# Optimization experiments

Hardware: AMD Instinct MI355X
Metric: run time of the kernel (lower is better)

## Reference

```python
import jax, jax.numpy as jnp
import numpy as np

N_NODES = 50000
D_IN = 256
D_OUT = 128
N_POS = 1600000   # positive edges used for GCN aggregation
N_PRED = 500000   # edges to score


def setup_inputs() -> dict:
    key = jax.random.key(0)
    ks = jax.random.split(key, 6)
    x = jax.random.normal(ks[0], (N_NODES, D_IN), dtype=jnp.float32)
    pos_edge_index = jax.random.randint(ks[1], (2, N_POS), 0, N_NODES)
    edge_index = jax.random.randint(ks[2], (2, N_PRED), 0, N_NODES)
    # init_linear: Linear(d_in, d_in); stored as (in, out) so fwd is x @ W1 + b1
    W1 = jax.random.normal(ks[3], (D_IN, D_IN), dtype=jnp.float32) / np.sqrt(D_IN).astype(np.float32)
    b1 = jnp.zeros((D_IN,), dtype=jnp.float32)
    # GCNConv weight (in, out) and bias
    Wc = jax.random.normal(ks[4], (D_IN, D_OUT), dtype=jnp.float32) / np.sqrt(D_IN).astype(np.float32)
    bc = jnp.zeros((D_OUT,), dtype=jnp.float32)
    return dict(x=x, edge_index=edge_index, pos_edge_index=pos_edge_index,
                W1=W1, b1=b1, Wc=Wc, bc=bc)


def reference(x, edge_index, pos_edge_index, W1, b1, Wc, bc):
    n = x.shape[0]
    # init_linear
    h = x @ W1 + b1                                  # [N, D_IN]
    # GCNConv: linear transform first, then normalized scatter-add aggregation
    h = h @ Wc                                       # [N, D_OUT]
    # add self-loops (PyG GCNConv default add_self_loops=True, edge_weight=1)
    loops = jnp.arange(n, dtype=pos_edge_index.dtype)
    row = jnp.concatenate([pos_edge_index[0], loops])  # source
    col = jnp.concatenate([pos_edge_index[1], loops])  # target (aggregation)
    # symmetric normalization: deg over target, norm = d^-1/2[row]*d^-1/2[col]
    deg = jax.ops.segment_sum(jnp.ones_like(col, dtype=h.dtype), col, num_segments=n)
    dinv = jnp.where(deg > 0, jax.lax.rsqrt(deg), 0.0)
    norm = dinv[row] * dinv[col]                     # [E+N]
    msgs = h[row] * norm[:, None]                    # gather + scale
    out = jax.ops.segment_sum(msgs, col, num_segments=n) + bc  # scatter-add + bias
    # edge dot-product scoring
    logits = (out[edge_index[0]] * out[edge_index[1]]).sum(axis=-1)  # [N_PRED]
    return logits
```

## Files before the change

### kernel.cpp

```cpp
#include <hip/hip_runtime.h>

#define N_NODES 50000
#define D_IN 256
#define D_OUT 128
#define N_POS 1600000
#define N_PRED 500000

#define G_BUCKETS 782
#define GPAD 1024
#define SB 640
#define CHUNK 2500
#define CAP 4096
#define GEMM_BLOCKS 782
#define QPRED 125000

typedef __attribute__((ext_vector_type(8))) short short8;
typedef __attribute__((ext_vector_type(4))) float f32x4;

__device__ __forceinline__ unsigned short f2bf(float f) {
    unsigned int u = __float_as_uint(f);
    u += 0x7FFFu + ((u >> 16) & 1u);
    return (unsigned short)(u >> 16);
}
__device__ __forceinline__ unsigned int pk2(float a, float b) {
    unsigned int ua = __float_as_uint(a), ub = __float_as_uint(b);
    ua += 0x7FFFu + ((ua >> 16) & 1u);
    ub += 0x7FFFu + ((ub >> 16) & 1u);
    return (ua >> 16) | (ub & 0xFFFF0000u);
}
__device__ __forceinline__ float bflo(unsigned int u) { return __uint_as_float(u << 16); }
__device__ __forceinline__ float bfhi(unsigned int u) { return __uint_as_float(u & 0xFFFF0000u); }

__device__ __forceinline__ float dot8(uint4 ua, uint4 ub) {
    return bflo(ua.x) * bflo(ub.x) + bfhi(ua.x) * bfhi(ub.x)
         + bflo(ua.y) * bflo(ub.y) + bfhi(ua.y) * bfhi(ub.y)
         + bflo(ua.z) * bflo(ub.z) + bfhi(ua.z) * bfhi(ub.z)
         + bflo(ua.w) * bflo(ub.w) + bfhi(ua.w) * bfhi(ub.w);
}

__global__ void fuse_weights_k(const float* __restrict__ W1, const float* __restrict__ Wc,
                               const float* __restrict__ b1,
                               unsigned short* __restrict__ Bp, float* __restrict__ bf,
                               int* __restrict__ bfill) {
    if (blockIdx.x == 128) {
        for (int g = threadIdx.x; g < G_BUCKETS; g += 256) bfill[g] = g * CAP;
        return;
    }
    int gid = blockIdx.x * blockDim.x + threadIdx.x;
    int k = gid >> 7;
    int n = gid & 127;
    float acc = 0.f;
    #pragma unroll 4
    for (int kk = 0; kk < D_IN; ++kk)
        acc += W1[k * D_IN + kk] * Wc[kk * D_OUT + n];
    int ks = k >> 5, q = (k >> 3) & 3, jj = k & 7;
    int nt = n >> 4, nl = n & 15;
    int lane = q * 16 + nl;
    Bp[(((long)(ks * 8 + nt)) * 64 + lane) * 8 + jj] = f2bf(acc);
    if (gid < D_OUT) {
        float accb = 0.f;
        for (int kk = 0; kk < D_IN; ++kk)
            accb += b1[kk] * Wc[kk * D_OUT + gid];
        bf[gid] = accb;
    }
}

__global__ __launch_bounds__(256) void scatter_gemm_k(const int* __restrict__ row,
                                                      const int* __restrict__ col,
                                                      int* __restrict__ bfill,
                                                      unsigned int* __restrict__ eb,
                                                      const float* __restrict__ x,
                                                      const uint4* __restrict__ Bp,
                                                      const float* __restrict__ bf,
                                                      unsigned short* __restrict__ hsb) {
    __shared__ __align__(16) char smem[27456];
    if (blockIdx.x < GEMM_BLOCKS) {
        const int wave = threadIdx.x >> 6;
        const int lane = threadIdx.x & 63;
        const int q    = lane >> 4;
        const int ml   = lane & 15;
        const int m0   = blockIdx.x * 64 + wave * 16;

        f32x4 acc[8];
        #pragma unroll
        for (int t = 0; t < 8; ++t) acc[t] = (f32x4){0.f, 0.f, 0.f, 0.f};

        long arow = m0 + ml; if (arow > N_NODES - 1) arow = N_NODES - 1;
        const float* xrow = x + arow * D_IN + q * 8;

        #pragma unroll
        for (int ks = 0; ks < 8; ++ks) {
            float4 xa = *(const float4*)(xrow + ks * 32);
            float4 xb = *(const float4*)(xrow + ks * 32 + 4);
            union { short8 s; unsigned int u[4]; } af;
            af.u[0] = pk2(xa.x, xa.y);
            af.u[1] = pk2(xa.z, xa.w);
            af.u[2] = pk2(xb.x, xb.y);
            af.u[3] = pk2(xb.z, xb.w);
            #pragma unroll
            for (int nt = 0; nt < 8; ++nt) {
                union { uint4 v; short8 s; } bu;
                bu.v = Bp[(long)(ks * 8 + nt) * 64 + lane];
                acc[nt] = __builtin_amdgcn_mfma_f32_16x16x32_bf16(af.s, bu.s, acc[nt], 0, 0, 0);
            }
        }

        unsigned short* o = (unsigned short*)smem + wave * 2048;
        #pragma unroll
        for (int nt = 0; nt < 8; ++nt) {
            float bn = bf[nt * 16 + ml];
            #pragma unroll
            for (int r = 0; r < 4; ++r) {
                float val = acc[nt][r] + bn;
                o[(q * 4 + r) * 128 + nt * 16 + ml] = f2bf(val);
            }
        }
        __syncthreads();
        #pragma unroll
        for (int i = 0; i < 4; ++i) {
            int fb = i * 1024 + lane * 16;
            int v = m0 + (fb >> 8);
            if (v < N_NODES) {
                uint4 val = *(const uint4*)((const char*)o + fb);
                *(uint4*)((char*)hsb + (long)v * 256 + (fb & 255)) = val;
            }
        }
    } else {
        int* hist  = (int*)smem;
        int* lofs  = hist + GPAD;
        int* fill2 = lofs + GPAD;
        int* base  = fill2 + GPAD;
        int* part  = base + GPAD;
        unsigned int* stag = (unsigned int*)(part + 256);
        int t = threadIdx.x;
        for (int i = t; i < GPAD; i += 256) { hist[i] = 0; fill2[i] = 0; }
        __syncthreads();
        int e0 = (blockIdx.x - GEMM_BLOCKS) * CHUNK;
        for (int i = t; i < CHUNK; i += 256)
            atomicAdd(&hist[col[e0 + i] >> 6], 1);
        __syncthreads();
        int h[4], p4 = 0;
        #pragma unroll
        for (int i = 0; i < 4; ++i) { h[i] = hist[4 * t + i]; p4 += h[i]; }
        part[t] = p4;
        __syncthreads();
        for (int d = 1; d < 256; d <<= 1) {
            int add = (t >= d) ? part[t - d] : 0;
            __syncthreads();
            part[t] += add;
            __syncthreads();
        }
        int ex = part[t] - p4;
        #pragma unroll
        for (int i = 0; i < 4; ++i) { lofs[4 * t + i] = ex; ex += h[i]; }
        __syncthreads();
        for (int g = t; g < G_BUCKETS; g += 256) {
            int c = hist[g];
            base[g] = c ? atomicAdd(&bfill[g], c) : 0;
        }
        for (int i = t; i < CHUNK; i += 256) {
            int c = col[e0 + i];
            int g = c >> 6;
            unsigned int u = (unsigned int)row[e0 + i] | ((unsigned int)(c & 63) << 16)
                           | ((unsigned int)g << 22);
            int lp = atomicAdd(&fill2[g], 1);
            stag[lofs[g] + lp] = u;
        }
        __syncthreads();
        for (int i = t; i < CHUNK; i += 256) {
            unsigned int u = stag[i];
            int g = u >> 22;
            eb[base[g] + (i - lofs[g])] = u;
        }
    }
}

__global__ __launch_bounds__(256) void csr_build_k(const int* __restrict__ bfill,
                                                   const unsigned int* __restrict__ eb,
                                                   unsigned short* __restrict__ csr,
                                                   int* __restrict__ offs,
                                                   int* __restrict__ ends,
                                                   float* __restrict__ dinv) {
    __shared__ unsigned int stag[CAP];
    __shared__ unsigned short stag2[CAP];
    __shared__ int hist[64], lofs[64], fill[64];
    int t = threadIdx.x;
    int g = blockIdx.x;
    int s = g * CAP;
    int cnt = bfill[g] - s;
    if (t < 64) { hist[t] = 0; fill[t] = 0; }
    __syncthreads();
    for (int i = t; i < cnt; i += 256) {
        unsigned int u = eb[s + i];
        stag[i] = u;
        atomicAdd(&hist[(u >> 16) & 63], 1);
    }
    __syncthreads();
    if (t == 0) {
        int run = 0;
        for (int k = 0; k < 64; ++k) { lofs[k] = run; run += hist[k]; }
    }
    __syncthreads();
    if (t < 64) {
        int v = g * 64 + t;
        if (v < N_NODES) {
            offs[v] = s + lofs[t];
            ends[v] = s + lofs[t] + hist[t];
            dinv[v] = rsqrtf((float)hist[t] + 1.0f);
        }
    }
    for (int i = t; i < cnt; i += 256) {
        unsigned int u = stag[i];
        int nl = (u >> 16) & 63;
        int lp = atomicAdd(&fill[nl], 1);
        stag2[lofs[nl] + lp] = (unsigned short)(u & 0xFFFF);
    }
    __syncthreads();
    for (int i = t; i < cnt; i += 256)
        csr[s + i] = stag2[i];
}

__global__ __launch_bounds__(256) void aggregate_csr_k(const int* __restrict__ offs,
                                                       const int* __restrict__ ends,
                                                       const unsigned short* __restrict__ csr,
                                                       const uint4* __restrict__ hs4,
                                                       const float* __restrict__ dinv,
                                                       const float* __restrict__ bc,
                                                       uint4* __restrict__ feat4) {
    int v    = blockIdx.x * 4 + (threadIdx.x >> 6);
    int lane = threadIdx.x & 63;
    int grp  = lane >> 4, li = lane & 15;
    int s0 = offs[v], s1 = ends[v];

    float a[8] = {0.f, 0.f, 0.f, 0.f, 0.f, 0.f, 0.f, 0.f};
    int i = s0 + grp;
    for (; i + 12 < s1; i += 16) {
        int r0 = csr[i], r1 = csr[i + 4], r2 = csr[i + 8], r3 = csr[i + 12];
        uint4 u0 = hs4[r0 * 16 + li];
        uint4 u1 = hs4[r1 * 16 + li];
        uint4 u2 = hs4[r2 * 16 + li];
        uint4 u3 = hs4[r3 * 16 + li];
        float d0 = dinv[r0], d1 = dinv[r1], d2 = dinv[r2], d3 = dinv[r3];
        a[0] = fmaf(d0, bflo(u0.x), a[0]); a[0] = fmaf(d1, bflo(u1.x), a[0]);
        a[0] = fmaf(d2, bflo(u2.x), a[0]); a[0] = fmaf(d3, bflo(u3.x), a[0]);
        a[1] = fmaf(d0, bfhi(u0.x), a[1]); a[1] = fmaf(d1, bfhi(u1.x), a[1]);
        a[1] = fmaf(d2, bfhi(u2.x), a[1]); a[1] = fmaf(d3, bfhi(u3.x), a[1]);
        a[2] = fmaf(d0, bflo(u0.y), a[2]); a[2] = fmaf(d1, bflo(u1.y), a[2]);
        a[2] = fmaf(d2, bflo(u2.y), a[2]); a[2] = fmaf(d3, bflo(u3.y), a[2]);
        a[3] = fmaf(d0, bfhi(u0.y), a[3]); a[3] = fmaf(d1, bfhi(u1.y), a[3]);
        a[3] = fmaf(d2, bfhi(u2.y), a[3]); a[3] = fmaf(d3, bfhi(u3.y), a[3]);
        a[4] = fmaf(d0, bflo(u0.z), a[4]); a[4] = fmaf(d1, bflo(u1.z), a[4]);
        a[4] = fmaf(d2, bflo(u2.z), a[4]); a[4] = fmaf(d3, bflo(u3.z), a[4]);
        a[5] = fmaf(d0, bfhi(u0.z), a[5]); a[5] = fmaf(d1, bfhi(u1.z), a[5]);
        a[5] = fmaf(d2, bfhi(u2.z), a[5]); a[5] = fmaf(d3, bfhi(u3.z), a[5]);
        a[6] = fmaf(d0, bflo(u0.w), a[6]); a[6] = fmaf(d1, bflo(u1.w), a[6]);
        a[6] = fmaf(d2, bflo(u2.w), a[6]); a[6] = fmaf(d3, bflo(u3.w), a[6]);
        a[7] = fmaf(d0, bfhi(u0.w), a[7]); a[7] = fmaf(d1, bfhi(u1.w), a[7]);
        a[7] = fmaf(d2, bfhi(u2.w), a[7]); a[7] = fmaf(d3, bfhi(u3.w), a[7]);
    }
    for (; i + 4 < s1; i += 8) {
        int r0 = csr[i], r1 = csr[i + 4];
        uint4 u0 = hs4[r0 * 16 + li];
        uint4 u1 = hs4[r1 * 16 + li];
        float d0 = dinv[r0], d1 = dinv[r1];
        a[0] = fmaf(d0, bflo(u0.x), a[0]); a[0] = fmaf(d1, bflo(u1.x), a[0]);
        a[1] = fmaf(d0, bfhi(u0.x), a[1]); a[1] = fmaf(d1, bfhi(u1.x), a[1]);
        a[2] = fmaf(d0, bflo(u0.y), a[2]); a[2] = fmaf(d1, bflo(u1.y), a[2]);
        a[3] = fmaf(d0, bfhi(u0.y), a[3]); a[3] = fmaf(d1, bfhi(u1.y), a[3]);
        a[4] = fmaf(d0, bflo(u0.z), a[4]); a[4] = fmaf(d1, bflo(u1.z), a[4]);
        a[5] = fmaf(d0, bfhi(u0.z), a[5]); a[5] = fmaf(d1, bfhi(u1.z), a[5]);
        a[6] = fmaf(d0, bflo(u0.w), a[6]); a[6] = fmaf(d1, bflo(u1.w), a[6]);
        a[7] = fmaf(d0, bfhi(u0.w), a[7]); a[7] = fmaf(d1, bfhi(u1.w), a[7]);
    }
    if (i < s1) {
        int r = csr[i];
        uint4 u = hs4[r * 16 + li];
        float d = dinv[r];
        a[0] = fmaf(d, bflo(u.x), a[0]); a[1] = fmaf(d, bfhi(u.x), a[1]);
        a[2] = fmaf(d, bflo(u.y), a[2]); a[3] = fmaf(d, bfhi(u.y), a[3]);
        a[4] = fmaf(d, bflo(u.z), a[4]); a[5] = fmaf(d, bfhi(u.z), a[5]);
        a[6] = fmaf(d, bflo(u.w), a[6]); a[7] = fmaf(d, bfhi(u.w), a[7]);
    }
    #pragma unroll
    for (int j = 0; j < 8; ++j) {
        a[j] += __shfl_xor(a[j], 16);
        a[j] += __shfl_xor(a[j], 32);
    }
    if (grp == 0) {
        uint4 su = hs4[v * 16 + li];
        float dv = dinv[v];
        float4 b0 = *(const float4*)(bc + li * 8);
        float4 b1 = *(const float4*)(bc + li * 8 + 4);
        float f0 = dv * (a[0] + dv * bflo(su.x)) + b0.x;
        float f1 = dv * (a[1] + dv * bfhi(su.x)) + b0.y;
        float f2 = dv * (a[2] + dv * bflo(su.y)) + b0.z;
        float f3 = dv * (a[3] + dv * bfhi(su.y)) + b0.w;
        float f4 = dv * (a[4] + dv * bflo(su.z)) + b1.x;
        float f5 = dv * (a[5] + dv * bfhi(su.z)) + b1.y;
        float f6 = dv * (a[6] + dv * bflo(su.w)) + b1.z;
        float f7 = dv * (a[7] + dv * bfhi(su.w)) + b1.w;
        uint4 o;
        o.x = pk2(f0, f1); o.y = pk2(f2, f3); o.z = pk2(f4, f5); o.w = pk2(f6, f7);
        feat4[v * 16 + li] = o;
    }
}

__global__ void score_k(const int* __restrict__ src, const int* __restrict__ dst,
                        const uint4* __restrict__ feat4, float* __restrict__ out) {
    int gid = blockIdx.x * blockDim.x + threadIdx.x;
    int e = gid >> 4;
    int c = gid & 15;
    if (e >= QPRED) return;
    int e0 = e, e1 = e + QPRED, e2 = e + 2 * QPRED, e3 = e + 3 * QPRED;
    int a0 = src[e0], b0 = dst[e0];
    int a1 = src[e1], b1 = dst[e1];
    int a2 = src[e2], b2 = dst[e2];
    int a3 = src[e3], b3 = dst[e3];
    uint4 ua0 = feat4[(long)a0 * 16 + c];
    uint4 ub0 = feat4[(long)b0 * 16 + c];
    uint4 ua1 = feat4[(long)a1 * 16 + c];
    uint4 ub1 = feat4[(long)b1 * 16 + c];
    uint4 ua2 = feat4[(long)a2 * 16 + c];
    uint4 ub2 = feat4[(long)b2 * 16 + c];
    uint4 ua3 = feat4[(long)a3 * 16 + c];
    uint4 ub3 = feat4[(long)b3 * 16 + c];
    float p0 = dot8(ua0, ub0);
    float p1 = dot8(ua1, ub1);
    float p2 = dot8(ua2, ub2);
    float p3 = dot8(ua3, ub3);
    #pragma unroll
    for (int m = 8; m; m >>= 1) {
        p0 += __shfl_xor(p0, m, 16);
        p1 += __shfl_xor(p1, m, 16);
        p2 += __shfl_xor(p2, m, 16);
        p3 += __shfl_xor(p3, m, 16);
    }
    if (c == 0) {
        out[e0] = p0;
        out[e1] = p1;
        out[e2] = p2;
        out[e3] = p3;
    }
}

extern "C" void kernel_launch(void* const* d_in, const int* in_sizes, int n_in,
                              void* d_out, int out_size, void* d_ws, size_t ws_size,
                              hipStream_t stream) {
    const float* x   = (const float*)d_in[0];
    const int*   ei  = (const int*)  d_in[1];
    const int*   pe  = (const int*)  d_in[2];
    const float* W1  = (const float*)d_in[3];
    const float* b1  = (const float*)d_in[4];
    const float* Wc  = (const float*)d_in[5];
    const float* bc  = (const float*)d_in[6];
    float* out = (float*)d_out;

    const int* pe_row = pe;
    const int* pe_col = pe + N_POS;
    const int* ei_src = ei;
    const int* ei_dst = ei + N_PRED;

    char* w = (char*)d_ws;
    unsigned short* Bp = (unsigned short*)w;  w += 32768 * 2;
    float* bf    = (float*)w;                 w += 128 * 4;
    float* dinv  = (float*)w;                 w += 50000 * 4;
    int*   bfill = (int*)w;                   w += GPAD * 4;
    int*   offs  = (int*)w;                   w += 50000 * 4;
    int*   ends  = (int*)w;                   w += 50000 * 4;
    unsigned int* eb = (unsigned int*)w;      w += (long)G_BUCKETS * CAP * 4;
    unsigned short* csr = (unsigned short*)w; w += (long)G_BUCKETS * CAP * 2;
    unsigned short* hsb   = (unsigned short*)w;  w += (long)N_NODES * D_OUT * 2;
    unsigned short* featb = (unsigned short*)w;

    fuse_weights_k<<<129, 256, 0, stream>>>(W1, Wc, b1, Bp, bf, bfill);

    scatter_gemm_k<<<GEMM_BLOCKS + SB, 256, 0, stream>>>(pe_row, pe_col, bfill, eb,
                                                         x, (const uint4*)Bp, bf, hsb);

    csr_build_k   <<<G_BUCKETS, 256, 0, stream>>>(bfill, eb, csr, offs, ends, dinv);

    aggregate_csr_k<<<N_NODES / 4, 256, 0, stream>>>(offs, ends, csr, (const uint4*)hsb,
                                                     dinv, bc, (uint4*)featb);

    score_k       <<<(QPRED * 16 + 255) / 256, 256, 0, stream>>>(
                      ei_src, ei_dst, (const uint4*)featb, out);
}
```

Measured before the change: 264.7 us.

## Partition CSR neighbor lists by source tile for cache-local aggregation

The CSR build now sorts each node's neighbors into four source-row tiles and records five offsets per node. The aggregation kernel processes 25 nodes per block and sweeps the tiles in order, keeping partial sums in shared memory. The aim is to keep the gathered hs rows within a smaller working set so they hit in cache. In exchange it adds a parallel prefix scan in the CSR build, per-tile loop overhead, shared-memory accumulation and a lower per-wave unroll depth.

```diff
diff --git a/kernel.cpp b/kernel.cpp
--- a/kernel.cpp
+++ b/kernel.cpp
@@ -13,6 +13,11 @@
 #define CAP 4096
 #define GEMM_BLOCKS 782
 #define QPRED 125000
+
+#define NT 4
+#define TSZ 12500
+#define NPB 25
+#define AGGB 2000
 
 typedef __attribute__((ext_vector_type(8))) short short8;
 typedef __attribute__((ext_vector_type(4))) float f32x4;
@@ -178,130 +183,141 @@
 __global__ __launch_bounds__(256) void csr_build_k(const int* __restrict__ bfill,
                                                    const unsigned int* __restrict__ eb,
                                                    unsigned short* __restrict__ csr,
-                                                   int* __restrict__ offs,
-                                                   int* __restrict__ ends,
+                                                   int* __restrict__ offs5,
                                                    float* __restrict__ dinv) {
     __shared__ unsigned int stag[CAP];
     __shared__ unsigned short stag2[CAP];
-    __shared__ int hist[64], lofs[64], fill[64];
+    __shared__ int hist[256], lofs[256], fill[256], part[256];
     int t = threadIdx.x;
     int g = blockIdx.x;
     int s = g * CAP;
     int cnt = bfill[g] - s;
-    if (t < 64) { hist[t] = 0; fill[t] = 0; }
+    hist[t] = 0; fill[t] = 0;
     __syncthreads();
     for (int i = t; i < cnt; i += 256) {
         unsigned int u = eb[s + i];
         stag[i] = u;
-        atomicAdd(&hist[(u >> 16) & 63], 1);
-    }
-    __syncthreads();
-    if (t == 0) {
-        int run = 0;
-        for (int k = 0; k < 64; ++k) { lofs[k] = run; run += hist[k]; }
-    }
+        int r = u & 0xFFFF;
+        int tile = (r >= TSZ) + (r >= 2 * TSZ) + (r >= 3 * TSZ);
+        atomicAdd(&hist[((u >> 16) & 63) * NT + tile], 1);
+    }
+    __syncthreads();
+    int hv = hist[t];
+    part[t] = hv;
+    __syncthreads();
+    for (int d = 1; d < 256; d <<= 1) {
+        int add = (t >= d) ? part[t - d] : 0;
+        __syncthreads();
+        part[t] += add;
+        __syncthreads();
+    }
+    lofs[t] = part[t] - hv;
     __syncthreads();
     if (t < 64) {
         int v = g * 64 + t;
         if (v < N_NODES) {
-            offs[v] = s + lofs[t];
-            ends[v] = s + lofs[t] + hist[t];
-            dinv[v] = rsqrtf((float)hist[t] + 1.0f);
+            int b4 = t * NT;
+            int o0 = s + lofs[b4];
+            int c0 = hist[b4], c1 = hist[b4 + 1], c2 = hist[b4 + 2], c3 = hist[b4 + 3];
+            offs5[v * 5 + 0] = o0;
+            offs5[v * 5 + 1] = o0 + c0;
+            offs5[v * 5 + 2] = o0 + c0 + c1;
+            offs5[v * 5 + 3] = o0 + c0 + c1 + c2;
+            offs5[v * 5 + 4] = o0 + c0 + c1 + c2 + c3;
+            dinv[v] = rsqrtf((float)(c0 + c1 + c2 + c3) + 1.0f);
         }
     }
     for (int i = t; i < cnt; i += 256) {
         unsigned int u = stag[i];
-        int nl = (u >> 16) & 63;
-        int lp = atomicAdd(&fill[nl], 1);
-        stag2[lofs[nl] + lp] = (unsigned short)(u & 0xFFFF);
+        int r = u & 0xFFFF;
+        int tile = (r >= TSZ) + (r >= 2 * TSZ) + (r >= 3 * TSZ);
+        int key = ((u >> 16) & 63) * NT + tile;
+        int lp = atomicAdd(&fill[key], 1);
+        stag2[lofs[key] + lp] = (unsigned short)r;
     }
     __syncthreads();
     for (int i = t; i < cnt; i += 256)
         csr[s + i] = stag2[i];
 }
 
-__global__ __launch_bounds__(256) void aggregate_csr_k(const int* __restrict__ offs,
-                                                       const int* __restrict__ ends,
+__global__ __launch_bounds__(256) void aggregate_csr_k(const int* __restrict__ offs5,
                                                        const unsigned short* __restrict__ csr,
                                                        const uint4* __restrict__ hs4,
                                                        const float* __restrict__ dinv,
                                                        const float* __restrict__ bc,
                                                        uint4* __restrict__ feat4) {
-    int v    = blockIdx.x * 4 + (threadIdx.x >> 6);
-    int lane = threadIdx.x & 63;
+    __shared__ float accs[NPB][128];
+    int tid  = threadIdx.x;
+    int wave = tid >> 6;
+    int lane = tid & 63;
     int grp  = lane >> 4, li = lane & 15;
-    int s0 = offs[v], s1 = ends[v];
-
-    float a[8] = {0.f, 0.f, 0.f, 0.f, 0.f, 0.f, 0.f, 0.f};
-    int i = s0 + grp;
-    for (; i + 12 < s1; i += 16) {
-        int r0 = csr[i], r1 = csr[i + 4], r2 = csr[i + 8], r3 = csr[i + 12];
-        uint4 u0 = hs4[r0 * 16 + li];
-        uint4 u1 = hs4[r1 * 16 + li];
-        uint4 u2 = hs4[r2 * 16 + li];
-        uint4 u3 = hs4[r3 * 16 + li];
-        float d0 = dinv[r0], d1 = dinv[r1], d2 = dinv[r2], d3 = dinv[r3];
-        a[0] = fmaf(d0, bflo(u0.x), a[0]); a[0] = fmaf(d1, bflo(u1.x), a[0]);
-        a[0] = fmaf(d2, bflo(u2.x), a[0]); a[0] = fmaf(d3, bflo(u3.x), a[0]);
-        a[1] = fmaf(d0, bfhi(u0.x), a[1]); a[1] = fmaf(d1, bfhi(u1.x), a[1]);
-        a[1] = fmaf(d2, bfhi(u2.x), a[1]); a[1] = fmaf(d3, bfhi(u3.x), a[1]);
-        a[2] = fmaf(d0, bflo(u0.y), a[2]); a[2] = fmaf(d1, bflo(u1.y), a[2]);
-        a[2] = fmaf(d2, bflo(u2.y), a[2]); a[2] = fmaf(d3, bflo(u3.y), a[2]);
-        a[3] = fmaf(d0, bfhi(u0.y), a[3]); a[3] = fmaf(d1, bfhi(u1.y), a[3]);
-        a[3] = fmaf(d2, bfhi(u2.y), a[3]); a[3] = fmaf(d3, bfhi(u3.y), a[3]);
-        a[4] = fmaf(d0, bflo(u0.z), a[4]); a[4] = fmaf(d1, bflo(u1.z), a[4]);
-        a[4] = fmaf(d2, bflo(u2.z), a[4]); a[4] = fmaf(d3, bflo(u3.z), a[4]);
-        a[5] = fmaf(d0, bfhi(u0.z), a[5]); a[5] = fmaf(d1, bfhi(u1.z), a[5]);
-        a[5] = fmaf(d2, bfhi(u2.z), a[5]); a[5] = fmaf(d3, bfhi(u3.z), a[5]);
-        a[6] = fmaf(d0, bflo(u0.w), a[6]); a[6] = fmaf(d1, bflo(u1.w), a[6]);
-        a[6] = fmaf(d2, bflo(u2.w), a[6]); a[6] = fmaf(d3, bflo(u3.w), a[6]);
-        a[7] = fmaf(d0, bfhi(u0.w), a[7]); a[7] = fmaf(d1, bfhi(u1.w), a[7]);
-        a[7] = fmaf(d2, bfhi(u2.w), a[7]); a[7] = fmaf(d3, bfhi(u3.w), a[7]);
-    }
-    for (; i + 4 < s1; i += 8) {
-        int r0 = csr[i], r1 = csr[i + 4];
-        uint4 u0 = hs4[r0 * 16 + li];
-        uint4 u1 = hs4[r1 * 16 + li];
-        float d0 = dinv[r0], d1 = dinv[r1];
-        a[0] = fmaf(d0, bflo(u0.x), a[0]); a[0] = fmaf(d1, bflo(u1.x), a[0]);
-        a[1] = fmaf(d0, bfhi(u0.x), a[1]); a[1] = fmaf(d1, bfhi(u1.x), a[1]);
-        a[2] = fmaf(d0, bflo(u0.y), a[2]); a[2] = fmaf(d1, bflo(u1.y), a[2]);
-        a[3] = fmaf(d0, bfhi(u0.y), a[3]); a[3] = fmaf(d1, bfhi(u1.y), a[3]);
-        a[4] = fmaf(d0, bflo(u0.z), a[4]); a[4] = fmaf(d1, bflo(u1.z), a[4]);
-        a[5] = fmaf(d0, bfhi(u0.z), a[5]); a[5] = fmaf(d1, bfhi(u1.z), a[5]);
-        a[6] = fmaf(d0, bflo(u0.w), a[6]); a[6] = fmaf(d1, bflo(u1.w), a[6]);
-        a[7] = fmaf(d0, bfhi(u0.w), a[7]); a[7] = fmaf(d1, bfhi(u1.w), a[7]);
-    }
-    if (i < s1) {
-        int r = csr[i];
-        uint4 u = hs4[r * 16 + li];
-        float d = dinv[r];
-        a[0] = fmaf(d, bflo(u.x), a[0]); a[1] = fmaf(d, bfhi(u.x), a[1]);
-        a[2] = fmaf(d, bflo(u.y), a[2]); a[3] = fmaf(d, bfhi(u.y), a[3]);
-        a[4] = fmaf(d, bflo(u.z), a[4]); a[5] = fmaf(d, bfhi(u.z), a[5]);
-        a[6] = fmaf(d, bflo(u.w), a[6]); a[7] = fmaf(d, bfhi(u.w), a[7]);
-    }
-    #pragma unroll
-    for (int j = 0; j < 8; ++j) {
-        a[j] += __shfl_xor(a[j], 16);
-        a[j] += __shfl_xor(a[j], 32);
-    }
-    if (grp == 0) {
-        uint4 su = hs4[v * 16 + li];
+    int vbase = blockIdx.x * NPB;
+
+    for (int i = tid; i < NPB * 128; i += 256) ((float*)accs)[i] = 0.f;
+    __syncthreads();
+
+    #pragma unroll 1
+    for (int tt = 0; tt < NT; ++tt) {
+        for (int n = wave; n < NPB; n += 4) {
+            int v = vbase + n;
+            int s0 = offs5[v * 5 + tt], s1 = offs5[v * 5 + tt + 1];
+            if (s0 == s1) continue;
+            float a[8] = {0.f, 0.f, 0.f, 0.f, 0.f, 0.f, 0.f, 0.f};
+            int i = s0 + grp;
+            for (; i + 4 < s1; i += 8) {
+                int r0 = csr[i], r1 = csr[i + 4];
+                uint4 u0 = hs4[r0 * 16 + li];
+                uint4 u1 = hs4[r1 * 16 + li];
+                float d0 = dinv[r0], d1 = dinv[r1];
+                a[0] = fmaf(d0, bflo(u0.x), a[0]); a[0] = fmaf(d1, bflo(u1.x), a[0]);
+                a[1] = fmaf(d0, bfhi(u0.x), a[1]); a[1] = fmaf(d1, bfhi(u1.x), a[1]);
+                a[2] = fmaf(d0, bflo(u0.y), a[2]); a[2] = fmaf(d1, bflo(u1.y), a[2]);
+                a[3] = fmaf(d0, bfhi(u0.y), a[3]); a[3] = fmaf(d1, bfhi(u1.y), a[3]);
+                a[4] = fmaf(d0, bflo(u0.z), a[4]); a[4] = fmaf(d1, bflo(u1.z), a[4]);
+                a[5] = fmaf(d0, bfhi(u0.z), a[5]); a[5] = fmaf(d1, bfhi(u1.z), a[5]);
+                a[6] = fmaf(d0, bflo(u0.w), a[6]); a[6] = fmaf(d1, bflo(u1.w), a[6]);
+                a[7] = fmaf(d0, bfhi(u0.w), a[7]); a[7] = fmaf(d1, bfhi(u1.w), a[7]);
+            }
+            if (i < s1) {
+                int r = csr[i];
+                uint4 u = hs4[r * 16 + li];
+                float d = dinv[r];
+                a[0] = fmaf(d, bflo(u.x), a[0]); a[1] = fmaf(d, bfhi(u.x), a[1]);
+                a[2] = fmaf(d, bflo(u.y), a[2]); a[3] = fmaf(d, bfhi(u.y), a[3]);
+                a[4] = fmaf(d, bflo(u.z), a[4]); a[5] = fmaf(d, bfhi(u.z), a[5]);
+                a[6] = fmaf(d, bflo(u.w), a[6]); a[7] = fmaf(d, bfhi(u.w), a[7]);
+            }
+            #pragma unroll
+            for (int j = 0; j < 8; ++j) {
+                a[j] += __shfl_xor(a[j], 16);
+                a[j] += __shfl_xor(a[j], 32);
+            }
+            if (grp == 0) {
+                #pragma unroll
+                for (int j = 0; j < 8; ++j) accs[n][li * 8 + j] += a[j];
+            }
+        }
+    }
+    __syncthreads();
+    int gid4 = wave * 4 + grp;
+    for (int n = gid4; n < NPB; n += 16) {
+        int v = vbase + n;
+        uint4 su = hs4[(long)v * 16 + li];
         float dv = dinv[v];
         float4 b0 = *(const float4*)(bc + li * 8);
         float4 b1 = *(const float4*)(bc + li * 8 + 4);
-        float f0 = dv * (a[0] + dv * bflo(su.x)) + b0.x;
-        float f1 = dv * (a[1] + dv * bfhi(su.x)) + b0.y;
-        float f2 = dv * (a[2] + dv * bflo(su.y)) + b0.z;
-        float f3 = dv * (a[3] + dv * bfhi(su.y)) + b0.w;
-        float f4 = dv * (a[4] + dv * bflo(su.z)) + b1.x;
-        float f5 = dv * (a[5] + dv * bfhi(su.z)) + b1.y;
-        float f6 = dv * (a[6] + dv * bflo(su.w)) + b1.z;
-        float f7 = dv * (a[7] + dv * bfhi(su.w)) + b1.w;
+        const float* ac = &accs[n][li * 8];
+        float f0 = dv * (ac[0] + dv * bflo(su.x)) + b0.x;
+        float f1 = dv * (ac[1] + dv * bfhi(su.x)) + b0.y;
+        float f2 = dv * (ac[2] + dv * bflo(su.y)) + b0.z;
+        float f3 = dv * (ac[3] + dv * bfhi(su.y)) + b0.w;
+        float f4 = dv * (ac[4] + dv * bflo(su.z)) + b1.x;
+        float f5 = dv * (ac[5] + dv * bfhi(su.z)) + b1.y;
+        float f6 = dv * (ac[6] + dv * bflo(su.w)) + b1.z;
+        float f7 = dv * (ac[7] + dv * bfhi(su.w)) + b1.w;
         uint4 o;
         o.x = pk2(f0, f1); o.y = pk2(f2, f3); o.z = pk2(f4, f5); o.w = pk2(f6, f7);
-        feat4[v * 16 + li] = o;
+        feat4[(long)v * 16 + li] = o;
     }
 }
 
@@ -365,8 +381,7 @@
     float* bf    = (float*)w;                 w += 128 * 4;
     float* dinv  = (float*)w;                 w += 50000 * 4;
     int*   bfill = (int*)w;                   w += GPAD * 4;
-    int*   offs  = (int*)w;                   w += 50000 * 4;
-    int*   ends  = (int*)w;                   w += 50000 * 4;
+    int*   offs5 = (int*)w;                   w += 50000 * 5 * 4;
     unsigned int* eb = (unsigned int*)w;      w += (long)G_BUCKETS * CAP * 4;
     unsigned short* csr = (unsigned short*)w; w += (long)G_BUCKETS * CAP * 2;
     unsigned short* hsb   = (unsigned short*)w;  w += (long)N_NODES * D_OUT * 2;
@@ -377,10 +392,10 @@
     scatter_gemm_k<<<GEMM_BLOCKS + SB, 256, 0, stream>>>(pe_row, pe_col, bfill, eb,
                                                          x, (const uint4*)Bp, bf, hsb);
 
-    csr_build_k   <<<G_BUCKETS, 256, 0, stream>>>(bfill, eb, csr, offs, ends, dinv);
-
-    aggregate_csr_k<<<N_NODES / 4, 256, 0, stream>>>(offs, ends, csr, (const uint4*)hsb,
-                                                     dinv, bc, (uint4*)featb);
+    csr_build_k   <<<G_BUCKETS, 256, 0, stream>>>(bfill, eb, csr, offs5, dinv);
+
+    aggregate_csr_k<<<AGGB, 256, 0, stream>>>(offs5, csr, (const uint4*)hsb,
+                                              dinv, bc, (uint4*)featb);
 
     score_k       <<<(QPRED * 16 + 255) / 256, 256, 0, stream>>>(
                       ei_src, ei_dst, (const uint4*)featb, out);
```

Measured after the change: 262.0 us. No clear change (-1.0%).
